# Performance work log

Hardware: AMD Instinct MI355X
Metric: run time of the kernel (lower is better)

The kernel has to match this reference:

```python
import jax, jax.numpy as jnp
import numpy as np

H = 1024
V = 50257


def setup_inputs() -> dict:
    key = jax.random.key(0)
    ks = jax.random.split(key, 10)
    s = 0.02
    return {
        "x": jax.random.randint(ks[0], (1,), 0, V, dtype=jnp.int32),
        "h0": jax.random.normal(ks[1], (1, 1, H), jnp.float32),
        "c0": jax.random.normal(ks[2], (1, 1, H), jnp.float32),
        "emb": jax.random.normal(ks[3], (V, H), jnp.float32) * s,
        "w_ih": jax.random.normal(ks[4], (4 * H, H), jnp.float32) * s,
        "w_hh": jax.random.normal(ks[5], (4 * H, H), jnp.float32) * s,
        "b_ih": jax.random.normal(ks[6], (4 * H,), jnp.float32) * s,
        "b_hh": jax.random.normal(ks[7], (4 * H,), jnp.float32) * s,
        "w_out": jax.random.normal(ks[8], (V, H), jnp.float32) * s,
        "b_out": jax.random.normal(ks[9], (V,), jnp.float32) * s,
    }


def reference(x, h0, c0, emb, w_ih, w_hh, b_ih, b_hh, w_out, b_out):
    # embedding lookup + view(1,1,-1) + relu -> [1, H]
    e = jax.nn.relu(emb[x].reshape(1, H))
    h = h0[0]  # [1, H]
    c = c0[0]  # [1, H]
    # single LSTM cell step; PyTorch gate order: i, f, g, o
    gates = e @ w_ih.T + b_ih + h @ w_hh.T + b_hh  # [1, 4H]
    i, f, g, o = jnp.split(gates, 4, axis=1)
    c_new = jax.nn.sigmoid(f) * c + jax.nn.sigmoid(i) * jnp.tanh(g)
    h_new = jax.nn.sigmoid(o) * jnp.tanh(c_new)
    # output projection + log-softmax over vocab
    logits = h_new @ w_out.T + b_out  # [1, V]
    out = jax.nn.log_softmax(logits, axis=1)
    return out, (h_new[None, :, :], c_new[None, :, :])
```

## Files before the change

kernel.cpp:

```cpp
#include <hip/hip_runtime.h>
#include <math.h>

#define HH 1024
#define VV 50257
#define NLB 2048

__device__ __forceinline__ float wave_reduce_sum(float v) {
#pragma unroll
    for (int off = 32; off > 0; off >>= 1) v += __shfl_down(v, off, 64);
    return v;
}

__device__ __forceinline__ void wave_reduce_lse(float& m, float& s) {
#pragma unroll
    for (int off = 32; off > 0; off >>= 1) {
        float om = __shfl_down(m, off, 64);
        float os = __shfl_down(s, off, 64);
        float M = fmaxf(m, om);
        s = s * expf(m - M) + os * expf(om - M);
        m = M;
    }
}

__device__ __forceinline__ float sigmoidf(float x) { return 1.0f / (1.0f + expf(-x)); }

__global__ __launch_bounds__(256) void k_gatecell(
    const int* __restrict__ x, const float* __restrict__ emb,
    const float* __restrict__ h0, const float* __restrict__ c0,
    const float* __restrict__ w_ih, const float* __restrict__ w_hh,
    const float* __restrict__ b_ih, const float* __restrict__ b_hh,
    float* __restrict__ out) {
    __shared__ float sg[4];
    int j = blockIdx.x;
    int w = threadIdx.x >> 6;
    int lane = threadIdx.x & 63;
    int row = w * HH + j;
    const float* e  = emb + (size_t)x[0] * HH;
    const float* wi = w_ih + (size_t)row * HH;
    const float* wh = w_hh + (size_t)row * HH;
    float acc = 0.0f;
#pragma unroll
    for (int k = 0; k < 4; ++k) {
        int idx = k * 256 + lane * 4;
        float4 wiv = *reinterpret_cast<const float4*>(wi + idx);
        float4 whv = *reinterpret_cast<const float4*>(wh + idx);
        float4 ev  = *reinterpret_cast<const float4*>(e + idx);
        float4 hv  = *reinterpret_cast<const float4*>(h0 + idx);
        ev.x = fmaxf(ev.x, 0.0f); ev.y = fmaxf(ev.y, 0.0f);
        ev.z = fmaxf(ev.z, 0.0f); ev.w = fmaxf(ev.w, 0.0f);
        acc += wiv.x * ev.x + wiv.y * ev.y + wiv.z * ev.z + wiv.w * ev.w;
        acc += whv.x * hv.x + whv.y * hv.y + whv.z * hv.z + whv.w * hv.w;
    }
    acc = wave_reduce_sum(acc);
    if (lane == 0) sg[w] = acc + b_ih[row] + b_hh[row];
    __syncthreads();
    if (threadIdx.x == 0) {
        float ig = sigmoidf(sg[0]);
        float fg = sigmoidf(sg[1]);
        float gg = tanhf(sg[2]);
        float og = sigmoidf(sg[3]);
        float c = fg * c0[j] + ig * gg;
        float h = og * tanhf(c);
        out[VV + j] = h;
        out[VV + HH + j] = c;
    }
}

__global__ __launch_bounds__(256) void k_logits_lse(
    const float* __restrict__ w_out, const float* __restrict__ b_out,
    const float* __restrict__ h, float* __restrict__ logits,
    float* __restrict__ pm, float* __restrict__ ps) {
    __shared__ float sm[4], ss[4];
    int w = threadIdx.x >> 6;
    int lane = threadIdx.x & 63;
    float m = -1e30f, s = 0.0f;
    for (int c = 0;; ++c) {
        int row = c * (NLB * 4) + blockIdx.x * 4 + w;
        if (row >= VV) break;
        const float* wr = w_out + (size_t)row * HH;
        float acc = 0.0f;
#pragma unroll
        for (int k = 0; k < 4; ++k) {
            int idx = k * 256 + lane * 4;
            float4 wv = *reinterpret_cast<const float4*>(wr + idx);
            float4 hv = *reinterpret_cast<const float4*>(h + idx);
            acc += wv.x * hv.x + wv.y * hv.y + wv.z * hv.z + wv.w * hv.w;
        }
        acc = wave_reduce_sum(acc);
        if (lane == 0) {
            float v = acc + b_out[row];
            logits[row] = v;
            if (v > m) {
                s = s * expf(m - v) + 1.0f;
                m = v;
            } else {
                s += expf(v - m);
            }
        }
    }
    if (lane == 0) { sm[w] = m; ss[w] = s; }
    __syncthreads();
    if (threadIdx.x == 0) {
        float M = sm[0], S = ss[0];
#pragma unroll
        for (int q = 1; q < 4; ++q) {
            float om = sm[q], os = ss[q];
            float MM = fmaxf(M, om);
            S = S * expf(M - MM) + os * expf(om - MM);
            M = MM;
        }
        pm[blockIdx.x] = M;
        ps[blockIdx.x] = S;
    }
}

__global__ __launch_bounds__(256) void k_final(
    const float* __restrict__ logits, const float* __restrict__ pm,
    const float* __restrict__ ps, float* __restrict__ out) {
    __shared__ float sm[4], ss[4];
    __shared__ float sZ;
    int tid = threadIdx.x;
    int lane = tid & 63;
    float m = -1e30f, s = 0.0f;
    for (int p = tid; p < NLB; p += 256) {
        float om = pm[p], os = ps[p];
        float M = fmaxf(m, om);
        s = s * expf(m - M) + os * expf(om - M);
        m = M;
    }
    wave_reduce_lse(m, s);
    if (lane == 0) { sm[tid >> 6] = m; ss[tid >> 6] = s; }
    __syncthreads();
    if (tid == 0) {
        float M = sm[0], S = ss[0];
#pragma unroll
        for (int q = 1; q < 4; ++q) {
            float om = sm[q], os = ss[q];
            float MM = fmaxf(M, om);
            S = S * expf(M - MM) + os * expf(om - MM);
            M = MM;
        }
        sZ = M + logf(S);
    }
    __syncthreads();
    float Z = sZ;
    for (int i = blockIdx.x * 256 + tid; i < VV; i += gridDim.x * 256)
        out[i] = logits[i] - Z;
}

extern "C" void kernel_launch(void* const* d_in, const int* in_sizes, int n_in,
                              void* d_out, int out_size, void* d_ws, size_t ws_size,
                              hipStream_t stream) {
    const int*   x     = (const int*)d_in[0];
    const float* h0    = (const float*)d_in[1];
    const float* c0    = (const float*)d_in[2];
    const float* emb   = (const float*)d_in[3];
    const float* w_ih  = (const float*)d_in[4];
    const float* w_hh  = (const float*)d_in[5];
    const float* b_ih  = (const float*)d_in[6];
    const float* b_hh  = (const float*)d_in[7];
    const float* w_out = (const float*)d_in[8];
    const float* b_out = (const float*)d_in[9];
    float* out = (float*)d_out;
    float* ws  = (float*)d_ws;

    float* logits = ws;
    float* pm     = ws + 50304;
    float* ps     = pm + NLB;

    k_gatecell<<<HH, 256, 0, stream>>>(x, emb, h0, c0, w_ih, w_hh, b_ih, b_hh, out);
    k_logits_lse<<<NLB, 256, 0, stream>>>(w_out, b_out, out + VV, logits, pm, ps);
    k_final<<<256, 256, 0, stream>>>(logits, pm, ps, out);
}
```

Baseline: 48.81 us.

## Unroll logits rows for more loads in flight, hoist h, split gate rows

The logits kernel now loads the hidden vector once per wave into registers, prefetches the bias values, and fully unrolls the row loop (six rows in pairs plus a guarded tail), so each wave has two rows of weight loads in flight at once. The gate kernel uses 512 threads, so each gate row is split across two waves with 8 contiguous floats per lane. The wave reductions switch to xor butterflies and the exp calls to the fast __expf intrinsic. This is meant to raise memory-level parallelism on the bandwidth-bound GEMV, at the cost of more registers and a hardcoded row count per wave that depends on VV and NWAVE.

New measurement: 47.41 us. 2.9% less time.

```diff
diff --git a/kernel.cpp b/kernel.cpp
--- a/kernel.cpp
+++ b/kernel.cpp
@@ -4,61 +4,68 @@
 #define HH 1024
 #define VV 50257
 #define NLB 2048
-
-__device__ __forceinline__ float wave_reduce_sum(float v) {
-#pragma unroll
-    for (int off = 32; off > 0; off >>= 1) v += __shfl_down(v, off, 64);
+#define NWAVE (NLB * 4)
+
+__device__ __forceinline__ float wave_allreduce_sum(float v) {
+#pragma unroll
+    for (int off = 1; off < 64; off <<= 1) v += __shfl_xor(v, off, 64);
     return v;
 }
 
-__device__ __forceinline__ void wave_reduce_lse(float& m, float& s) {
-#pragma unroll
-    for (int off = 32; off > 0; off >>= 1) {
-        float om = __shfl_down(m, off, 64);
-        float os = __shfl_down(s, off, 64);
-        float M = fmaxf(m, om);
-        s = s * expf(m - M) + os * expf(om - M);
-        m = M;
-    }
-}
-
-__device__ __forceinline__ float sigmoidf(float x) { return 1.0f / (1.0f + expf(-x)); }
-
-__global__ __launch_bounds__(256) void k_gatecell(
+__device__ __forceinline__ void lse_comb(float& m, float& s, float om, float os) {
+    float M = fmaxf(m, om);
+    s = s * __expf(m - M) + os * __expf(om - M);
+    m = M;
+}
+
+__device__ __forceinline__ float sigmoidf(float x) { return 1.0f / (1.0f + __expf(-x)); }
+
+__device__ __forceinline__ float dot4(float4 a, float4 b) {
+    return a.x * b.x + a.y * b.y + a.z * b.z + a.w * b.w;
+}
+
+__global__ __launch_bounds__(512) void k_gatecell(
     const int* __restrict__ x, const float* __restrict__ emb,
     const float* __restrict__ h0, const float* __restrict__ c0,
     const float* __restrict__ w_ih, const float* __restrict__ w_hh,
     const float* __restrict__ b_ih, const float* __restrict__ b_hh,
     float* __restrict__ out) {
-    __shared__ float sg[4];
-    int j = blockIdx.x;
-    int w = threadIdx.x >> 6;
-    int lane = threadIdx.x & 63;
-    int row = w * HH + j;
-    const float* e  = emb + (size_t)x[0] * HH;
-    const float* wi = w_ih + (size_t)row * HH;
-    const float* wh = w_hh + (size_t)row * HH;
-    float acc = 0.0f;
-#pragma unroll
-    for (int k = 0; k < 4; ++k) {
-        int idx = k * 256 + lane * 4;
-        float4 wiv = *reinterpret_cast<const float4*>(wi + idx);
-        float4 whv = *reinterpret_cast<const float4*>(wh + idx);
-        float4 ev  = *reinterpret_cast<const float4*>(e + idx);
-        float4 hv  = *reinterpret_cast<const float4*>(h0 + idx);
-        ev.x = fmaxf(ev.x, 0.0f); ev.y = fmaxf(ev.y, 0.0f);
-        ev.z = fmaxf(ev.z, 0.0f); ev.w = fmaxf(ev.w, 0.0f);
-        acc += wiv.x * ev.x + wiv.y * ev.y + wiv.z * ev.z + wiv.w * ev.w;
-        acc += whv.x * hv.x + whv.y * hv.y + whv.z * hv.z + whv.w * hv.w;
-    }
-    acc = wave_reduce_sum(acc);
-    if (lane == 0) sg[w] = acc + b_ih[row] + b_hh[row];
+    __shared__ float sg2[8];
+    const int j = blockIdx.x;
+    const int w = threadIdx.x >> 6;
+    const int lane = threadIdx.x & 63;
+    const int g = w >> 1, hf = w & 1;
+    const int row = g * HH + j;
+    const int base = hf * 512 + lane * 8;
+
+    const float* e  = emb + (size_t)x[0] * HH + base;
+    const float* wi = w_ih + (size_t)row * HH + base;
+    const float* wh = w_hh + (size_t)row * HH + base;
+    const float* hp = h0 + base;
+
+    float4 wi0 = *reinterpret_cast<const float4*>(wi);
+    float4 wi1 = *reinterpret_cast<const float4*>(wi + 4);
+    float4 wh0 = *reinterpret_cast<const float4*>(wh);
+    float4 wh1 = *reinterpret_cast<const float4*>(wh + 4);
+    float4 e0  = *reinterpret_cast<const float4*>(e);
+    float4 e1  = *reinterpret_cast<const float4*>(e + 4);
+    float4 hv0 = *reinterpret_cast<const float4*>(hp);
+    float4 hv1 = *reinterpret_cast<const float4*>(hp + 4);
+    e0.x = fmaxf(e0.x, 0.f); e0.y = fmaxf(e0.y, 0.f);
+    e0.z = fmaxf(e0.z, 0.f); e0.w = fmaxf(e0.w, 0.f);
+    e1.x = fmaxf(e1.x, 0.f); e1.y = fmaxf(e1.y, 0.f);
+    e1.z = fmaxf(e1.z, 0.f); e1.w = fmaxf(e1.w, 0.f);
+
+    float acc = dot4(wi0, e0) + dot4(wi1, e1) + dot4(wh0, hv0) + dot4(wh1, hv1);
+    acc = wave_allreduce_sum(acc);
+    if (lane == 0)
+        sg2[w] = acc + (hf == 0 ? b_ih[row] + b_hh[row] : 0.0f);
     __syncthreads();
     if (threadIdx.x == 0) {
-        float ig = sigmoidf(sg[0]);
-        float fg = sigmoidf(sg[1]);
-        float gg = tanhf(sg[2]);
-        float og = sigmoidf(sg[3]);
+        float ig = sigmoidf(sg2[0] + sg2[1]);
+        float fg = sigmoidf(sg2[2] + sg2[3]);
+        float gg = tanhf(sg2[4] + sg2[5]);
+        float og = sigmoidf(sg2[6] + sg2[7]);
         float c = fg * c0[j] + ig * gg;
         float h = og * tanhf(c);
         out[VV + j] = h;
@@ -71,44 +78,77 @@
     const float* __restrict__ h, float* __restrict__ logits,
     float* __restrict__ pm, float* __restrict__ ps) {
     __shared__ float sm[4], ss[4];
-    int w = threadIdx.x >> 6;
-    int lane = threadIdx.x & 63;
+    const int w = threadIdx.x >> 6;
+    const int lane = threadIdx.x & 63;
+    const int wid = blockIdx.x * 4 + w;
+
+    const float* hp = h + lane * 4;
+    float4 h0v = *reinterpret_cast<const float4*>(hp);
+    float4 h1v = *reinterpret_cast<const float4*>(hp + 256);
+    float4 h2v = *reinterpret_cast<const float4*>(hp + 512);
+    float4 h3v = *reinterpret_cast<const float4*>(hp + 768);
+
+    float bo[7];
+#pragma unroll
+    for (int c = 0; c < 6; ++c) bo[c] = b_out[wid + c * NWAVE];
+    {
+        int r6 = wid + 6 * NWAVE;
+        bo[6] = (r6 < VV) ? b_out[r6] : 0.0f;
+    }
+
+    const float* wb = w_out + (size_t)wid * HH + lane * 4;
     float m = -1e30f, s = 0.0f;
-    for (int c = 0;; ++c) {
-        int row = c * (NLB * 4) + blockIdx.x * 4 + w;
-        if (row >= VV) break;
-        const float* wr = w_out + (size_t)row * HH;
-        float acc = 0.0f;
-#pragma unroll
-        for (int k = 0; k < 4; ++k) {
-            int idx = k * 256 + lane * 4;
-            float4 wv = *reinterpret_cast<const float4*>(wr + idx);
-            float4 hv = *reinterpret_cast<const float4*>(h + idx);
-            acc += wv.x * hv.x + wv.y * hv.y + wv.z * hv.z + wv.w * hv.w;
+
+#pragma unroll
+    for (int c = 0; c < 6; c += 2) {
+        const float* pa = wb + (size_t)c * NWAVE * HH;
+        const float* pb = pa + (size_t)NWAVE * HH;
+        float4 a0 = *reinterpret_cast<const float4*>(pa);
+        float4 a1 = *reinterpret_cast<const float4*>(pa + 256);
+        float4 a2 = *reinterpret_cast<const float4*>(pa + 512);
+        float4 a3 = *reinterpret_cast<const float4*>(pa + 768);
+        float4 b0 = *reinterpret_cast<const float4*>(pb);
+        float4 b1 = *reinterpret_cast<const float4*>(pb + 256);
+        float4 b2 = *reinterpret_cast<const float4*>(pb + 512);
+        float4 b3 = *reinterpret_cast<const float4*>(pb + 768);
+        float accA = dot4(a0, h0v) + dot4(a1, h1v) + dot4(a2, h2v) + dot4(a3, h3v);
+        float accB = dot4(b0, h0v) + dot4(b1, h1v) + dot4(b2, h2v) + dot4(b3, h3v);
+        accA = wave_allreduce_sum(accA);
+        accB = wave_allreduce_sum(accB);
+        float vA = accA + bo[c];
+        float vB = accB + bo[c + 1];
+        if (lane == 0) {
+            logits[wid + c * NWAVE] = vA;
+            logits[wid + (c + 1) * NWAVE] = vB;
         }
-        acc = wave_reduce_sum(acc);
-        if (lane == 0) {
-            float v = acc + b_out[row];
-            logits[row] = v;
-            if (v > m) {
-                s = s * expf(m - v) + 1.0f;
-                m = v;
-            } else {
-                s += expf(v - m);
-            }
+        if (vA > m) { s = s * __expf(m - vA) + 1.0f; m = vA; }
+        else        { s += __expf(vA - m); }
+        if (vB > m) { s = s * __expf(m - vB) + 1.0f; m = vB; }
+        else        { s += __expf(vB - m); }
+    }
+    {
+        int row = wid + 6 * NWAVE;
+        if (row < VV) {
+            const float* pa = wb + (size_t)6 * NWAVE * HH;
+            float4 a0 = *reinterpret_cast<const float4*>(pa);
+            float4 a1 = *reinterpret_cast<const float4*>(pa + 256);
+            float4 a2 = *reinterpret_cast<const float4*>(pa + 512);
+            float4 a3 = *reinterpret_cast<const float4*>(pa + 768);
+            float acc = dot4(a0, h0v) + dot4(a1, h1v) + dot4(a2, h2v) + dot4(a3, h3v);
+            acc = wave_allreduce_sum(acc);
+            float v = acc + bo[6];
+            if (lane == 0) logits[row] = v;
+            if (v > m) { s = s * __expf(m - v) + 1.0f; m = v; }
+            else       { s += __expf(v - m); }
         }
     }
+
     if (lane == 0) { sm[w] = m; ss[w] = s; }
     __syncthreads();
     if (threadIdx.x == 0) {
         float M = sm[0], S = ss[0];
 #pragma unroll
-        for (int q = 1; q < 4; ++q) {
-            float om = sm[q], os = ss[q];
-            float MM = fmaxf(M, om);
-            S = S * expf(M - MM) + os * expf(om - MM);
-            M = MM;
-        }
+        for (int q = 1; q < 4; ++q) lse_comb(M, S, sm[q], ss[q]);
         pm[blockIdx.x] = M;
         ps[blockIdx.x] = S;
     }
@@ -123,23 +163,20 @@
     int lane = tid & 63;
     float m = -1e30f, s = 0.0f;
     for (int p = tid; p < NLB; p += 256) {
-        float om = pm[p], os = ps[p];
-        float M = fmaxf(m, om);
-        s = s * expf(m - M) + os * expf(om - M);
-        m = M;
-    }
-    wave_reduce_lse(m, s);
+        lse_comb(m, s, pm[p], ps[p]);
+    }
+#pragma unroll
+    for (int off = 1; off < 64; off <<= 1) {
+        float om = __shfl_xor(m, off, 64);
+        float os = __shfl_xor(s, off, 64);
+        lse_comb(m, s, om, os);
+    }
     if (lane == 0) { sm[tid >> 6] = m; ss[tid >> 6] = s; }
     __syncthreads();
     if (tid == 0) {
         float M = sm[0], S = ss[0];
 #pragma unroll
-        for (int q = 1; q < 4; ++q) {
-            float om = sm[q], os = ss[q];
-            float MM = fmaxf(M, om);
-            S = S * expf(M - MM) + os * expf(om - MM);
-            M = MM;
-        }
+        for (int q = 1; q < 4; ++q) lse_comb(M, S, sm[q], ss[q]);
         sZ = M + logf(S);
     }
     __syncthreads();
@@ -168,7 +205,7 @@
     float* pm     = ws + 50304;
     float* ps     = pm + NLB;
 
-    k_gatecell<<<HH, 256, 0, stream>>>(x, emb, h0, c0, w_ih, w_hh, b_ih, b_hh, out);
+    k_gatecell<<<HH, 512, 0, stream>>>(x, emb, h0, c0, w_ih, w_hh, b_ih, b_hh, out);
     k_logits_lse<<<NLB, 256, 0, stream>>>(w_out, b_out, out + VV, logits, pm, ps);
     k_final<<<256, 256, 0, stream>>>(logits, pm, ps, out);
 }
```
